# Optimization experiments

Hardware: AMD Instinct MI355X
Metric: run time of the kernel (lower is better)

The kernel has to match this reference:

```python
import jax, jax.numpy as jnp
import numpy as np
import math

N, K, M = 4, 3, 3
OUTC, INC = 64, 64

def _valid_combos():
    combos = []
    for n in range(1, N + 1):
        for k in range(K):
            for m in range(-M, M + 1):
                if abs(m) <= k and k < n:
                    combos.append((n, k, m))
    return combos

COMBOS = _valid_combos()  # 23 (n,k,m) triples, static


def _assoc_laguerre(k, a, x):
    # L_k^a(x) = sum_{i=0}^k (-1)^i C(k+a, k-i) x^i / i!  (static small degree)
    out = jnp.zeros_like(x)
    for i in range(k + 1):
        c = ((-1) ** i) * math.comb(k + a, k - i) / math.factorial(i)
        out = out + jnp.asarray(c, x.dtype) * x ** i
    return out


def _assoc_legendre(l, m, ct, st):
    # P_l^m(cos t) with Condon-Shortley phase; ct=cos t, st=sin t >= 0
    if m > 0:
        dfact = math.prod(range(1, 2 * m, 2))  # (2m-1)!!
        pmm = jnp.asarray(((-1) ** m) * dfact, ct.dtype) * st ** m
    else:
        pmm = jnp.ones_like(ct)
    if l == m:
        return pmm
    pmmp1 = ct * (2 * m + 1) * pmm
    if l == m + 1:
        return pmmp1
    for ll in range(m + 2, l + 1):
        pll = ((2 * ll - 1) * ct * pmmp1 - (ll + m - 1) * pmm) / (ll - m)
        pmm, pmmp1 = pmmp1, pll
    return pmmp1


def _hwfr(n, l, m, r, ct, st, phi):
    # real hydrogen-like wavefunction psi_{n,l,m}(r,theta,phi), a0 = 1
    rho = 2.0 * r / n
    norm_r = math.sqrt((2.0 / n) ** 3 * math.factorial(n - l - 1) / (2 * n * math.factorial(n + l)))
    R = norm_r * jnp.exp(-0.5 * rho) * rho ** l * _assoc_laguerre(n - l - 1, 2 * l + 1, rho)
    am = abs(m)
    Klm = math.sqrt((2 * l + 1) / (4 * math.pi) * math.factorial(l - am) / math.factorial(l + am))
    P = _assoc_legendre(l, am, ct, st)
    if m > 0:
        Y = math.sqrt(2.0) * Klm * jnp.cos(am * phi) * P
    elif m < 0:
        Y = math.sqrt(2.0) * Klm * jnp.sin(am * phi) * P
    else:
        Y = Klm * P
    return R * Y


def setup_inputs() -> dict:
    key = jax.random.key(0)
    k1, k2 = jax.random.split(key)
    position = jax.random.normal(k1, (8, 4096, 3), dtype=jnp.float32)
    coefficients = jax.random.normal(k2, (OUTC, INC, len(COMBOS)), dtype=jnp.float32)
    return {"position": position, "coefficients": coefficients}


def reference(position, coefficients):
    x, y, z = position[..., 0], position[..., 1], position[..., 2]
    r = jnp.sqrt(x * x + y * y + z * z) + 1e-12
    ct = z / r
    st = jnp.sqrt(jnp.clip(1.0 - ct * ct, 0.0, None))
    phi = jnp.arctan2(y, x)
    # (B, P, n_basis) -- loop over the small static basis set, not data dims
    poly = jnp.stack([_hwfr(n, l, m, r, ct, st, phi) for (n, l, m) in COMBOS], axis=-1)
    # einsum 'ijk, mnk -> mnij' as in the torch module -> (OutC, InC, B, P)
    return jnp.einsum('ijk,mnk->mnij', poly, coefficients)
```

## Files before the change

kernel.cpp:

```cpp
#include <hip/hip_runtime.h>
#include <math.h>

#define NPTS  32768
#define NPAIR 4096
#define NC    23
#define TPB   256
#define PPT   2
#define PTS_PER_BLOCK (TPB * PPT)
#define PT    64
#define NCP   24

namespace cgen {
constexpr double PI = 3.14159265358979323846264338327950288;
constexpr double fact(int n) { double r = 1; for (int i = 2; i <= n; ++i) r *= i; return r; }
constexpr double comb(int n, int k) { double r = 1; for (int i = 0; i < k; ++i) r = r * (n - i) / (i + 1); return r; }
constexpr double csqrt(double x) { double g = x > 1 ? x : 1.0; for (int i = 0; i < 100; ++i) g = 0.5 * (g + x / g); return g; }

struct Tables {
  int n[NC]; int l[NC]; int m[NC];
  double pref[NC];
  double lag[NC][4];
};
constexpr Tables gen() {
  Tables t{};
  int idx = 0;
  for (int n = 1; n <= 4; ++n)
    for (int k = 0; k < 3; ++k)
      for (int m = -3; m <= 3; ++m) {
        int am = m < 0 ? -m : m;
        if (!(am <= k && k < n)) continue;
        t.n[idx] = n; t.l[idx] = k; t.m[idx] = m;
        double norm_r = csqrt((2.0 / n) * (2.0 / n) * (2.0 / n) * fact(n - k - 1) / (2.0 * n * fact(n + k)));
        double Klm = csqrt((2.0 * k + 1.0) / (4.0 * PI) * fact(k - am) / fact(k + am));
        t.pref[idx] = norm_r * Klm * (m != 0 ? csqrt(2.0) : 1.0);
        int kk = n - k - 1, a = 2 * k + 1;
        for (int i = 0; i < 4; ++i) t.lag[idx][i] = 0.0;
        for (int i = 0; i <= kk; ++i)
          t.lag[idx][i] = ((i & 1) ? -1.0 : 1.0) * comb(kk + a, kk - i) / fact(i);
        ++idx;
      }
  return t;
}
constexpr Tables T = gen();
}

__global__ __launch_bounds__(TPB, 4)
void dcconv_poly_einsum(const float* __restrict__ pos,
                        const float* __restrict__ coef,
                        float* __restrict__ out) {
  __shared__ __align__(16) float lc[(PT + 1) * NCP];

  const int tid   = threadIdx.x;
  const int pt0   = blockIdx.x * PTS_PER_BLOCK + tid * PPT;
  const int pair0 = blockIdx.y * PT;

  {
    const float* __restrict__ cb = coef + (size_t)pair0 * NC;
#pragma unroll
    for (int i = tid; i < PT * NC; i += TPB) {
      const int row = i / NC;
      const int col = i - row * NC;
      lc[row * NCP + col] = cb[i];
    }
  }

  const float2* __restrict__ pv = reinterpret_cast<const float2*>(pos + (size_t)pt0 * 3);
  const float2 f0 = pv[0], f1 = pv[1], f2 = pv[2];

  float p0[NC], p1[NC];

  auto evalpt = [&](float x, float y, float z, float (&pc)[NC]) {
    const float rxy2 = x * x + y * y;
    const float r    = sqrtf(rxy2 + z * z) + 1e-12f;
    const float ct   = z / r;
    const float st   = sqrtf(rxy2) / r;
    const float st2  = st * st;
    const float invq = rsqrtf(fmaxf(rxy2, 1e-30f));
    const float cp   = x * invq;
    const float sp   = y * invq;
    const float c2p  = (cp - sp) * (cp + sp);
    const float s2p  = 2.0f * sp * cp;

    float rho[5]; rho[0] = 0.0f; rho[1] = 2.0f * r; rho[2] = r; rho[3] = (2.0f / 3.0f) * r; rho[4] = 0.5f * r;
    float en[5];  en[0] = 0.0f;
    en[4] = expf(-0.25f * r);
    en[2] = en[4] * en[4];
    en[1] = en[2] * en[2];
    en[3] = expf(-(1.0f / 3.0f) * r);

    float P[3][3] = {};
    P[0][0] = 1.0f;
    P[1][0] = ct;                    P[1][1] = -st;
    P[2][0] = 1.5f * ct * ct - 0.5f; P[2][1] = -3.0f * ct * st; P[2][2] = 3.0f * st2;

    float trig[5]; trig[0] = s2p; trig[1] = sp; trig[2] = 1.0f; trig[3] = cp; trig[4] = c2p;

#pragma unroll
    for (int c = 0; c < NC; ++c) {
      const int n = cgen::T.n[c], l = cgen::T.l[c], m = cgen::T.m[c];
      const int am = m < 0 ? -m : m;
      const float rh = rho[n];
      const float L = (float)cgen::T.lag[c][0]
                    + rh * ((float)cgen::T.lag[c][1]
                    + rh * ((float)cgen::T.lag[c][2]
                    + rh *  (float)cgen::T.lag[c][3]));
      const float rl = (l == 0) ? 1.0f : ((l == 1) ? rh : rh * rh);
      pc[c] = (float)cgen::T.pref[c] * en[n] * rl * L * P[l][am] * trig[m + 2];
    }
  };

  evalpt(f0.x, f0.y, f1.x, p0);
  evalpt(f1.y, f2.x, f2.y, p1);

  __syncthreads();

  const float4* __restrict__ lrow = reinterpret_cast<const float4*>(lc);
  float* __restrict__ optr = out + (size_t)pair0 * NPTS + pt0;

#define G4(CV, B)                                                  \
  a0 = fmaf(CV.x, p0[(B)+0], a0); a1 = fmaf(CV.x, p1[(B)+0], a1);  \
  a0 = fmaf(CV.y, p0[(B)+1], a0); a1 = fmaf(CV.y, p1[(B)+1], a1);  \
  a0 = fmaf(CV.z, p0[(B)+2], a0); a1 = fmaf(CV.z, p1[(B)+2], a1);  \
  a0 = fmaf(CV.w, p0[(B)+3], a0); a1 = fmaf(CV.w, p1[(B)+3], a1);

#define G3(CV, B)                                                  \
  a0 = fmaf(CV.x, p0[(B)+0], a0); a1 = fmaf(CV.x, p1[(B)+0], a1);  \
  a0 = fmaf(CV.y, p0[(B)+1], a0); a1 = fmaf(CV.y, p1[(B)+1], a1);  \
  a0 = fmaf(CV.z, p0[(B)+2], a0); a1 = fmaf(CV.z, p1[(B)+2], a1);

  float4 c0 = lrow[0], c1 = lrow[1], c2 = lrow[2],
         c3 = lrow[3], c4 = lrow[4], c5 = lrow[5];

#pragma unroll 4
  for (int j = 0; j < PT; ++j) {
    const float4* nrow = lrow + 6 * (j + 1);
    const float4 n0 = nrow[0], n1 = nrow[1], n2 = nrow[2],
                 n3 = nrow[3], n4 = nrow[4], n5 = nrow[5];

    float a0 = 0.0f, a1 = 0.0f;
    G4(c0, 0) G4(c1, 4) G4(c2, 8) G4(c3, 12) G4(c4, 16) G3(c5, 20)

    float2 res; res.x = a0; res.y = a1;
    *reinterpret_cast<float2*>(optr) = res;
    optr += NPTS;

    c0 = n0; c1 = n1; c2 = n2; c3 = n3; c4 = n4; c5 = n5;
  }
#undef G4
#undef G3
}

extern "C" void kernel_launch(void* const* d_in, const int* in_sizes, int n_in,
                              void* d_out, int out_size, void* d_ws, size_t ws_size,
                              hipStream_t stream) {
  const float* pos  = (const float*)d_in[0];
  const float* coef = (const float*)d_in[1];
  float* out = (float*)d_out;

  dim3 grid(NPTS / PTS_PER_BLOCK, NPAIR / PT);
  dim3 block(TPB);
  hipLaunchKernelGGL(dcconv_poly_einsum, grid, block, 0, stream, pos, coef, out);
}
```

Baseline: 540.1 us.

## Stream coefficient rows through scalar loads instead of LDS staging

Drops the shared-memory staging of the 64x23 coefficient tile and the block barrier. Each wave now reads coefficient rows directly into scalar registers with inline s_load_dwordx16/x8, double-buffered so the next row's load overlaps the current dot product. The dot product is split into even/odd accumulators to shorten dependency chains. This puts the kernel's correctness and ordering on hand-written asm waitcnt gates and scheduling barriers, and depends on the row addresses being wave-uniform.

```diff
diff --git a/kernel.cpp b/kernel.cpp
--- a/kernel.cpp
+++ b/kernel.cpp
@@ -8,7 +8,6 @@
 #define PPT   2
 #define PTS_PER_BLOCK (TPB * PPT)
 #define PT    64
-#define NCP   24
 
 namespace cgen {
 constexpr double PI = 3.14159265358979323846264338327950288;
@@ -44,25 +43,25 @@
 constexpr Tables T = gen();
 }
 
+typedef float f16v __attribute__((ext_vector_type(16)));
+typedef float f8v  __attribute__((ext_vector_type(8)));
+
+__device__ __forceinline__ void sload_row(const float* p, f16v& a, f8v& b) {
+  asm volatile("s_load_dwordx16 %0, %2, 0x0\n\t"
+               "s_load_dwordx8  %1, %2, 0x3c"
+               : "=&s"(a), "=&s"(b)
+               : "s"(p));
+}
+
+#define GATE(A, B) asm volatile("s_waitcnt lgkmcnt(0)" : "+s"(A), "+s"(B))
+
 __global__ __launch_bounds__(TPB, 4)
 void dcconv_poly_einsum(const float* __restrict__ pos,
                         const float* __restrict__ coef,
                         float* __restrict__ out) {
-  __shared__ __align__(16) float lc[(PT + 1) * NCP];
-
   const int tid   = threadIdx.x;
   const int pt0   = blockIdx.x * PTS_PER_BLOCK + tid * PPT;
   const int pair0 = blockIdx.y * PT;
-
-  {
-    const float* __restrict__ cb = coef + (size_t)pair0 * NC;
-#pragma unroll
-    for (int i = tid; i < PT * NC; i += TPB) {
-      const int row = i / NC;
-      const int col = i - row * NC;
-      lc[row * NCP + col] = cb[i];
-    }
-  }
 
   const float2* __restrict__ pv = reinterpret_cast<const float2*>(pos + (size_t)pt0 * 3);
   const float2 f0 = pv[0], f1 = pv[1], f2 = pv[2];
@@ -112,42 +111,50 @@
   evalpt(f0.x, f0.y, f1.x, p0);
   evalpt(f1.y, f2.x, f2.y, p1);
 
-  __syncthreads();
+  float* optr = out + (size_t)pair0 * NPTS + pt0;
 
-  const float4* __restrict__ lrow = reinterpret_cast<const float4*>(lc);
-  float* __restrict__ optr = out + (size_t)pair0 * NPTS + pt0;
-
-#define G4(CV, B)                                                  \
-  a0 = fmaf(CV.x, p0[(B)+0], a0); a1 = fmaf(CV.x, p1[(B)+0], a1);  \
-  a0 = fmaf(CV.y, p0[(B)+1], a0); a1 = fmaf(CV.y, p1[(B)+1], a1);  \
-  a0 = fmaf(CV.z, p0[(B)+2], a0); a1 = fmaf(CV.z, p1[(B)+2], a1);  \
-  a0 = fmaf(CV.w, p0[(B)+3], a0); a1 = fmaf(CV.w, p1[(B)+3], a1);
-
-#define G3(CV, B)                                                  \
-  a0 = fmaf(CV.x, p0[(B)+0], a0); a1 = fmaf(CV.x, p1[(B)+0], a1);  \
-  a0 = fmaf(CV.y, p0[(B)+1], a0); a1 = fmaf(CV.y, p1[(B)+1], a1);  \
-  a0 = fmaf(CV.z, p0[(B)+2], a0); a1 = fmaf(CV.z, p1[(B)+2], a1);
-
-  float4 c0 = lrow[0], c1 = lrow[1], c2 = lrow[2],
-         c3 = lrow[3], c4 = lrow[4], c5 = lrow[5];
-
-#pragma unroll 4
-  for (int j = 0; j < PT; ++j) {
-    const float4* nrow = lrow + 6 * (j + 1);
-    const float4 n0 = nrow[0], n1 = nrow[1], n2 = nrow[2],
-                 n3 = nrow[3], n4 = nrow[4], n5 = nrow[5];
-
-    float a0 = 0.0f, a1 = 0.0f;
-    G4(c0, 0) G4(c1, 4) G4(c2, 8) G4(c3, 12) G4(c4, 16) G3(c5, 20)
-
-    float2 res; res.x = a0; res.y = a1;
+  auto dot_store = [&](const f16v& CA, const f8v& CB) {
+    float e0 = 0.f, o0 = 0.f, e1 = 0.f, o1 = 0.f;
+#pragma unroll
+    for (int c = 0; c < 16; c += 2) {
+      e0 = fmaf(CA[c],     p0[c],     e0);
+      e1 = fmaf(CA[c],     p1[c],     e1);
+      o0 = fmaf(CA[c + 1], p0[c + 1], o0);
+      o1 = fmaf(CA[c + 1], p1[c + 1], o1);
+    }
+#pragma unroll
+    for (int c = 16; c < NC; c += 2) {
+      e0 = fmaf(CB[c - 15], p0[c], e0);
+      e1 = fmaf(CB[c - 15], p1[c], e1);
+      if (c + 1 < NC) {
+        o0 = fmaf(CB[c - 14], p0[c + 1], o0);
+        o1 = fmaf(CB[c - 14], p1[c + 1], o1);
+      }
+    }
+    float2 res; res.x = e0 + o0; res.y = e1 + o1;
     *reinterpret_cast<float2*>(optr) = res;
     optr += NPTS;
+  };
 
-    c0 = n0; c1 = n1; c2 = n2; c3 = n3; c4 = n4; c5 = n5;
+  const float* rp = coef + (size_t)pair0 * NC;
+  f16v A0, B0; f8v A1, B1;
+  sload_row(rp, A0, A1);
+
+#pragma unroll 1
+  for (int j = 0; j < PT; j += 2) {
+    GATE(A0, A1);
+    sload_row(rp + NC, B0, B1);
+    __builtin_amdgcn_sched_barrier(0);
+    dot_store(A0, A1);
+
+    GATE(B0, B1);
+    const float* rpn = rp + ((j + 2 < PT) ? 2 * NC : NC);
+    sload_row(rpn, A0, A1);
+    __builtin_amdgcn_sched_barrier(0);
+    dot_store(B0, B1);
+    rp = rpn;
   }
-#undef G4
-#undef G3
+  asm volatile("s_waitcnt lgkmcnt(0)");
 }
 
 extern "C" void kernel_launch(void* const* d_in, const int* in_sizes, int n_in,
```

Result: slower. 581.5 us (+7.7%).
